# Optimization experiments

Measured on AMD Instinct MI355X. Metric: run time of the kernel, lower is better.

Reference implementation:

```python
import jax, jax.numpy as jnp
import numpy as np

EPS = 1e-5
NB, NP, NA, NROT = 16, 1024, 12, 60
C0, C1 = 64, 128
CIN, CFEAT, COUT = 256, 512, 256


def _bn(x, g, b):
    # training-mode BatchNorm1d: stats over batch (+ spatial) dims, channel dim 1
    axes = (0,) if x.ndim == 2 else (0, 2)
    m = x.mean(axis=axes, keepdims=True)
    v = x.var(axis=axes, keepdims=True)
    sh = [1] * x.ndim; sh[1] = -1
    return (x - m) * jax.lax.rsqrt(v + EPS) * g.reshape(sh) + b.reshape(sh)


def _hat(v):  # (n,3) -> (n,3,3) skew-symmetric
    z = jnp.zeros_like(v[:, 0])
    return jnp.stack([z, -v[:, 2], v[:, 1],
                      v[:, 2], z, -v[:, 0],
                      -v[:, 1], v[:, 0], z], axis=-1).reshape(-1, 3, 3)


def _exp_so3(v):  # Rodrigues formula, (n,3) -> (n,3,3)
    theta = jnp.linalg.norm(v, axis=-1, keepdims=True)  # (n,1)
    k = v / jnp.where(theta < 1e-8, 1.0, theta)
    K = _hat(k)
    s = jnp.sin(theta)[..., None]
    c = (1.0 - jnp.cos(theta))[..., None]
    I = jnp.eye(3, dtype=v.dtype)
    return I + s * K + c * (K @ K)


def _pointnet(xyz, feats, W, b, g, bb):
    # PointnetSO3Conv: concat xyz (expanded over anchors) with feats, 1x1 conv, max over points
    nb, _, npts, na = feats.shape
    x = jnp.concatenate([jnp.broadcast_to(xyz[:, :, :, None], (nb, 3, npts, na)), feats], axis=1)
    y = jnp.einsum('oc,bcpa->bopa', W, x) + b[None, :, None, None]
    y = y.max(axis=2)  # max over points -> (nb, o, na)
    return jax.nn.relu(_bn(y, g, bb))


def setup_inputs() -> dict:
    key = jax.random.key(0)
    ks = iter(jax.random.split(key, 64))
    def nrm(shape, s=0.1):
        return jax.random.normal(next(ks), shape, dtype=jnp.float32) * s
    d = {
        'xyz0': nrm((NB, 3, NP), 1.0),
        'feats0': nrm((NB, C0, NP, NA), 1.0),
        'xyz1': nrm((NB, 3, NP), 1.0),
        'feats1': nrm((NB, C1, NP, NA), 1.0),
        'trace_idx': jax.random.randint(next(ks), (NA, NROT), 0, NA),
        'anchors': nrm((NROT, 3, 3), 1.0),
        'pn0_W': nrm((C0, C0 + 3)), 'pn0_b': nrm((C0,)), 'pn0_g': jnp.ones((C0,), jnp.float32), 'pn0_bb': jnp.zeros((C0,), jnp.float32),
        'pn1_W': nrm((C1, C1 + 3)), 'pn1_b': nrm((C1,)), 'pn1_g': jnp.ones((C1,), jnp.float32), 'pn1_bb': jnp.zeros((C1,), jnp.float32),
        'lin_W': nrm((CIN, C0 + C1)), 'lin_b': nrm((CIN,)), 'lin_g': jnp.ones((CIN,), jnp.float32), 'lin_bb': jnp.zeros((CIN,), jnp.float32),
        'feat_W': nrm((CFEAT, CIN * NA)), 'feat_b': nrm((CFEAT,)), 'feat_g': jnp.ones((CFEAT,), jnp.float32), 'feat_bb': jnp.zeros((CFEAT,), jnp.float32),
        'att_W1': nrm((128, CFEAT)), 'att_b1': nrm((128,)), 'att_g': jnp.ones((128,), jnp.float32), 'att_bb': jnp.zeros((128,), jnp.float32),
        'att_W2': nrm((1, 128)), 'att_b2': nrm((1,)),
        'reg_W1': nrm((128, CFEAT)), 'reg_b1': nrm((128,)), 'reg_g': jnp.ones((128,), jnp.float32), 'reg_bb': jnp.zeros((128,), jnp.float32),
        'reg_W2': nrm((7, 128)), 'reg_b2': nrm((7,)),
        'out_W1': nrm((CFEAT, CFEAT)), 'out_b1': nrm((CFEAT,)), 'out_g': jnp.ones((CFEAT,), jnp.float32), 'out_bb': jnp.zeros((CFEAT,), jnp.float32),
        'out_W2': nrm((COUT, CFEAT)), 'out_b2': nrm((COUT,)),
    }
    return d


def reference(xyz0, feats0, xyz1, feats1, trace_idx, anchors,
              pn0_W, pn0_b, pn0_g, pn0_bb, pn1_W, pn1_b, pn1_g, pn1_bb,
              lin_W, lin_b, lin_g, lin_bb, feat_W, feat_b, feat_g, feat_bb,
              att_W1, att_b1, att_g, att_bb, att_W2, att_b2,
              reg_W1, reg_b1, reg_g, reg_bb, reg_W2, reg_b2,
              out_W1, out_b1, out_g, out_bb, out_W2, out_b2):
    nb = feats0.shape[0]
    # _pooling: per-level pointnet + BN + relu, concat, pn_linear + pn_bn
    p0 = _pointnet(xyz0, feats0, pn0_W, pn0_b, pn0_g, pn0_bb)
    p1 = _pointnet(xyz1, feats1, pn1_W, pn1_b, pn1_g, pn1_bb)
    x = jnp.concatenate([p0, p1], axis=1)                                   # (nb, 192, na)
    x = _bn(jnp.einsum('oc,bca->boa', lin_W, x) + lin_b[None, :, None], lin_g, lin_bb)  # (nb,256,na)
    # gather trace_idx_ori and flatten channel x anchor dims
    x = x[:, :, trace_idx].reshape(nb, CIN * NA, NROT)                      # (nb,3072,60)
    xf = jax.nn.relu(_bn(jnp.einsum('oc,bca->boa', feat_W, x) + feat_b[None, :, None], feat_g, feat_bb))  # (nb,512,60)
    h = jax.nn.relu(_bn(jnp.einsum('oc,bca->boa', reg_W1, xf) + reg_b1[None, :, None], reg_g, reg_bb))
    residual = (jnp.einsum('oc,bca->boa', reg_W2, h) + reg_b2[None, :, None]).transpose(0, 2, 1)  # (nb,60,7)
    res_D = residual[:, :, :3] / jnp.linalg.norm(residual[:, :, :3], axis=-1, keepdims=True)
    res_N = (jax.nn.sigmoid(residual[:, :, 3]) - 0.5) * jnp.pi / 5
    res_V = res_D * res_N[..., None]
    res_R = _exp_so3(res_V.reshape(-1, 3)).reshape(nb, NROT, 3, 3)
    res_T = residual[:, :, 4:]
    pred_R = jnp.einsum('tij,btjk->btik', anchors, res_R)
    # attention head + softmax over 60 rotations
    a = jax.nn.relu(_bn(jnp.einsum('oc,bca->boa', att_W1, xf) + att_b1[None, :, None], att_g, att_bb))
    logits = (jnp.einsum('oc,bca->boa', att_W2, a) + att_b2[None, :, None])[:, 0]   # (nb,60)
    x_attn = jax.nn.softmax(logits, axis=-1)
    # max-pool over rotations + out MLP
    xm = xf.max(axis=-1)                                                    # (nb,512)
    o = jax.nn.relu(_bn(xm @ out_W1.T + out_b1, out_g, out_bb))
    x_out = o @ out_W2.T + out_b2
    return (x_out, x_attn, pred_R, res_T)
```

## Files before the change

### kernel.cpp

```cpp
#include <hip/hip_runtime.h>
#include <math.h>

#define NBATCH 16
#define NPTS   1024
#define NANG   12
#define NROTS  60
#define EPSV   1e-5f

#define WB0_OFF   0
#define WB1_OFF   3072
#define PART0_OFF 13312
#define PART1_OFF 799744
#define XF_OFF    13312
#define XM_OFF    504832
#define OACT_OFF  513024
#define XCAT_OFF  2372608
#define XLIN_OFF  2409472
#define XG_OFF    2458624
#define BRP_OFF   2458624
#define HACT_OFF  4424704
#define AACT_OFF  4547584
#define FRAW_OFF  5407744
#define FEATW_OFF 6882304

#define OUT_XOUT 0
#define OUT_ATTN 4096
#define OUT_PRED 5056
#define OUT_REST 13696

typedef short  bf16x8 __attribute__((ext_vector_type(8)));
typedef float  f32x4  __attribute__((ext_vector_type(4)));

__device__ __forceinline__ unsigned short f2bf_rne(float x){
  unsigned int u = __float_as_uint(x);
  u += 0x7FFFu + ((u >> 16) & 1u);
  return (unsigned short)(u >> 16);
}
__device__ __forceinline__ float bf2f(unsigned short h){
  return __uint_as_float(((unsigned int)h) << 16);
}

__device__ __forceinline__ bf16x8 pack8(const float* f){
  union { unsigned int u[4]; bf16x8 v; } r;
  #pragma unroll
  for (int i = 0; i < 4; i++)
    r.u[i] = __builtin_amdgcn_perm(__float_as_uint(f[2*i+1]),
                                   __float_as_uint(f[2*i]), 0x07060302u);
  return r.v;
}

__device__ __forceinline__ void stage16(const unsigned short* g, unsigned short* l){
  __builtin_amdgcn_global_load_lds((const __attribute__((address_space(1))) void*)g,
                                   (__attribute__((address_space(3))) void*)l, 16, 0, 0);
}

template<int NT>
__device__ __forceinline__ void block_stats(float v, float& m, float& var, float* sbuf){
  constexpr int NW = NT / 64;
  float s = v, s2 = v * v;
  #pragma unroll
  for (int off = 32; off; off >>= 1){
    s  += __shfl_xor(s,  off, 64);
    s2 += __shfl_xor(s2, off, 64);
  }
  const int w = threadIdx.x >> 6;
  if ((threadIdx.x & 63) == 0){ sbuf[w] = s; sbuf[NW + w] = s2; }
  __syncthreads();
  float ts = 0.f, ts2 = 0.f;
  #pragma unroll
  for (int i = 0; i < NW; i++){ ts += sbuf[i]; ts2 += sbuf[NW + i]; }
  m = ts / (float)NT;
  var = ts2 / (float)NT - m * m;
}

template<int C>
__device__ __forceinline__ void prep_wb_body(int idx, const float* __restrict__ W,
                                             unsigned short* __restrict__ Wb){
  constexpr int KPAD = C + 32;
  if (idx >= C * KPAD) return;
  const int o = idx / KPAD, k = idx % KPAD;
  float v = 0.f;
  if (k < C)          v = W[(size_t)o * (C + 3) + 3 + k];
  else if (k < C + 3) v = W[(size_t)o * (C + 3) + (k - C)];
  Wb[idx] = f2bf_rne(v);
}

__global__ __launch_bounds__(256) void prep_all(
    const float* __restrict__ W0, const float* __restrict__ W1,
    const float* __restrict__ FW,
    unsigned short* __restrict__ wb0, unsigned short* __restrict__ wb1,
    unsigned short* __restrict__ fw2){
  const int blk = blockIdx.x;
  if (blk < 24){
    prep_wb_body<64>(blk * 256 + threadIdx.x, W0, wb0);
  } else if (blk < 104){
    prep_wb_body<128>((blk - 24) * 256 + threadIdx.x, W1, wb1);
  } else {
    const int idx = (blk - 104) * 256 + threadIdx.x;
    const int o = idx / 3072, k = idx % 3072;
    const float x = FW[idx];
    const unsigned short hi = f2bf_rne(x);
    const unsigned short lo = f2bf_rne(x - bf2f(hi));
    fw2[(size_t)o * 6144 + k] = hi;
    fw2[(size_t)o * 6144 + 3072 + k] = lo;
  }
}

#define SROW 196
template<int C>
__device__ __forceinline__ void pn_body(
    const float* __restrict__ xyz, const float* __restrict__ feats,
    const unsigned short* __restrict__ Wb, float* __restrict__ part,
    float* Bs ){
  constexpr int KPAD = C + 32;
  constexpr int NFK  = C / 32;
  constexpr int MT   = C / 16;
  const int nchunk = blockIdx.x, b = blockIdx.y;
  const int tid  = threadIdx.x;
  const int lane = tid & 63, wave = tid >> 6;
  const int g = lane >> 4, l16 = lane & 15;
  const int colbase = wave * 48;
  const int nbase   = nchunk * 192;

  int nn[3], pp[3];
  #pragma unroll
  for (int t = 0; t < 3; t++){
    nn[t] = colbase + t * 16 + l16;
    pp[t] = (nbase + nn[t]) / 12;
  }

  f32x4 acc[MT][3];
  #pragma unroll
  for (int m = 0; m < MT; m++)
    #pragma unroll
    for (int t = 0; t < 3; t++)
      acc[m][t] = (f32x4){0.f, 0.f, 0.f, 0.f};

  const float* fB = feats + (size_t)b * C * (NPTS * NANG) + nbase;

  int srow[6], scol[6], sslot[6];
  #pragma unroll
  for (int jj = 0; jj < 6; jj++){
    const int idx = tid + 256 * jj;
    srow[jj]  = idx / 48;
    scol[jj]  = (idx % 48) * 4;
    sslot[jj] = (srow[jj] & 7) * 4 + (srow[jj] >> 3);
  }

  {
    float4 v[6];
    #pragma unroll
    for (int jj = 0; jj < 6; jj++)
      v[jj] = *(const float4*)(fB + (size_t)srow[jj] * (NPTS * NANG) + scol[jj]);
    #pragma unroll
    for (int jj = 0; jj < 6; jj++)
      *(float4*)(&Bs[sslot[jj] * SROW + scol[jj]]) = v[jj];
  }
  __syncthreads();

  #pragma unroll
  for (int ks = 0; ks < NFK; ks++){
    float* Bc = Bs + (ks & 1) * (32 * SROW);
    float* Bn = Bs + ((ks & 1) ^ 1) * (32 * SROW);
    float4 v[6];
    if (ks + 1 < NFK){
      const int kb = (ks + 1) * 32;
      #pragma unroll
      for (int jj = 0; jj < 6; jj++)
        v[jj] = *(const float4*)(fB + (size_t)(kb + srow[jj]) * (NPTS * NANG) + scol[jj]);
    }
    const int kb = ks * 32;
    bf16x8 Bf[3];
    #pragma unroll
    for (int t = 0; t < 3; t++){
      float f[8];
      #pragma unroll
      for (int j = 0; j < 8; j++)
        f[j] = Bc[(j * 4 + g) * SROW + nn[t]];
      Bf[t] = pack8(f);
    }
    #pragma unroll
    for (int m = 0; m < MT; m++){
      const bf16x8 Af = *(const bf16x8*)(Wb + (size_t)(m * 16 + l16) * KPAD + kb + g * 8);
      #pragma unroll
      for (int t = 0; t < 3; t++)
        acc[m][t] = __builtin_amdgcn_mfma_f32_16x16x32_bf16(Af, Bf[t], acc[m][t], 0, 0, 0);
    }
    if (ks + 1 < NFK){
      #pragma unroll
      for (int jj = 0; jj < 6; jj++)
        *(float4*)(&Bn[sslot[jj] * SROW + scol[jj]]) = v[jj];
    }
    __syncthreads();
  }

  {
    const int kb = C;
    bf16x8 Bf[3];
    #pragma unroll
    for (int t = 0; t < 3; t++){
      float f[8];
      #pragma unroll
      for (int j = 0; j < 8; j++) f[j] = 0.f;
      if (g == 0){
        #pragma unroll
        for (int j = 0; j < 3; j++)
          f[j] = xyz[(size_t)(b * 3 + j) * NPTS + pp[t]];
      }
      Bf[t] = pack8(f);
    }
    #pragma unroll
    for (int m = 0; m < MT; m++){
      const bf16x8 Af = *(const bf16x8*)(Wb + (size_t)(m * 16 + l16) * KPAD + kb + g * 8);
      #pragma unroll
      for (int t = 0; t < 3; t++)
        acc[m][t] = __builtin_amdgcn_mfma_f32_16x16x32_bf16(Af, Bf[t], acc[m][t], 0, 0, 0);
    }
  }

  float* yb = Bs;
  #pragma unroll
  for (int m = 0; m < MT; m++){
    __syncthreads();
    #pragma unroll
    for (int t = 0; t < 3; t++)
      #pragma unroll
      for (int r = 0; r < 4; r++)
        yb[(g * 4 + r) * SROW + nn[t]] = acc[m][t][r];
    __syncthreads();
    if (tid < 192){
      const int o_l = tid / 12, a = tid % 12;
      float mx = -3.4e38f;
      #pragma unroll
      for (int pl = 0; pl < 16; pl++)
        mx = fmaxf(mx, yb[o_l * SROW + pl * 12 + a]);
      part[((size_t)(b * 64 + nchunk) * C + m * 16 + o_l) * 12 + a] = mx;
    }
  }
}

__global__ __launch_bounds__(256) void pn_both(
    const float* __restrict__ xyz0, const float* __restrict__ feats0,
    const unsigned short* __restrict__ wb0, float* __restrict__ part0,
    const float* __restrict__ xyz1, const float* __restrict__ feats1,
    const unsigned short* __restrict__ wb1, float* __restrict__ part1){
  __shared__ float Bs[2 * 32 * SROW];
  if (blockIdx.z == 0) pn_body<64> (xyz0, feats0, wb0, part0, Bs);
  else                 pn_body<128>(xyz1, feats1, wb1, part1, Bs);
}

__global__ void pn_reduce_bn(const float* __restrict__ part0, const float* __restrict__ part1,
    const float* __restrict__ b0, const float* __restrict__ g0, const float* __restrict__ bb0,
    const float* __restrict__ b1, const float* __restrict__ g1, const float* __restrict__ bb1,
    float* __restrict__ xcat){
  const int ch = blockIdx.x, t = threadIdx.x;
  const int b = t / 12, a = t % 12;
  const float* part; const float *bias, *g, *bb; int o, Cl;
  if (ch < 64){ part = part0; bias = b0; g = g0; bb = bb0; o = ch;      Cl = 64;  }
  else        { part = part1; bias = b1; g = g1; bb = bb1; o = ch - 64; Cl = 128; }
  const float* pp = part + ((size_t)(b * 64) * Cl + o) * 12 + a;
  const size_t kstride = (size_t)Cl * 12;
  float v = pp[0];
  for (int k = 1; k < 64; k++) v = fmaxf(v, pp[(size_t)k * kstride]);
  v += bias[o];
  __shared__ float sbuf[8];
  float m, var;
  block_stats<192>(v, m, var, sbuf);
  float xn = (v - m) * rsqrtf(var + EPSV) * g[o] + bb[o];
  xcat[((size_t)b * 192 + ch) * 12 + a] = fmaxf(xn, 0.f);
}

__global__ void lin_bn(const float* __restrict__ xcat, const float* __restrict__ W,
    const float* __restrict__ bias, const float* __restrict__ g, const float* __restrict__ bb,
    float* __restrict__ xlin){
  const int o = blockIdx.x, t = threadIdx.x;
  const int b = t / 12, a = t % 12;
  const float* xr = xcat + (size_t)b * 2304 + a;
  const float* wr = W + (size_t)o * 192;
  float v = bias[o];
  for (int c = 0; c < 192; c++) v = fmaf(wr[c], xr[(size_t)c * 12], v);
  __shared__ float sbuf[8];
  float m, var;
  block_stats<192>(v, m, var, sbuf);
  xlin[((size_t)b * 256 + o) * 12 + a] = (v - m) * rsqrtf(var + EPSV) * g[o] + bb[o];
}

__global__ void prep_xg(const float* __restrict__ xlin, const int* __restrict__ trace,
                        unsigned short* __restrict__ Xg){
  const int n = blockIdx.x;
  const int b = n / 60, r = n % 60;
  unsigned short* row = Xg + (size_t)n * 6144;
  __shared__ int ta[12];
  if (threadIdx.x < 12) ta[threadIdx.x] = trace[threadIdx.x * 60 + r];
  __syncthreads();
  for (int i = threadIdx.x; i < 3072; i += 256){
    const int c = i / 12, a = i % 12;
    const float x = xlin[((size_t)b * 256 + c) * 12 + ta[a]];
    const unsigned short hi = f2bf_rne(x);
    const unsigned short lo = f2bf_rne(x - bf2f(hi));
    row[i] = hi;
    row[3072 + i] = lo;
  }
}

__global__ __launch_bounds__(256) void feat_mfma(
    const unsigned short* __restrict__ Wb2, const unsigned short* __restrict__ Xg,
    float* __restrict__ fraw){
  const int nblk = blockIdx.x, mblk = blockIdx.y, seg = blockIdx.z;
  const int tid = threadIdx.x;
  const int lane = tid & 63, wave = tid >> 6;
  const int g = lane >> 4, l16 = lane & 15;
  const int kA = (seg == 1) ? 3072 : 0;
  const int kB = (seg == 2) ? 3072 : 0;
  const int sw = l16 & 7;
  const int wm = wave >> 1, wn = wave & 1;

  __shared__ unsigned short As[2][64 * 64];
  __shared__ unsigned short Bs[2][64 * 64];

  int rowj[2], colj[2], ldsoff[2];
  #pragma unroll
  for (int j = 0; j < 2; j++){
    const int idx = j * 256 + wave * 64 + lane;
    rowj[j]   = idx >> 3;
    colj[j]   = ((idx & 7) ^ (rowj[j] & 7)) * 8;
    ldsoff[j] = (j * 256 + wave * 64) * 8;
  }
  const unsigned short* Agb = Wb2 + (size_t)mblk * 64 * 6144 + kA;
  const unsigned short* Bgb = Xg  + (size_t)nblk * 64 * 6144 + kB;

  f32x4 acc[2][2];
  #pragma unroll
  for (int i = 0; i < 2; i++)
    #pragma unroll
    for (int j = 0; j < 2; j++)
      acc[i][j] = (f32x4){0.f, 0.f, 0.f, 0.f};

  #pragma unroll
  for (int j = 0; j < 2; j++){
    stage16(Agb + (size_t)rowj[j] * 6144 + colj[j], &As[0][ldsoff[j]]);
    stage16(Bgb + (size_t)rowj[j] * 6144 + colj[j], &Bs[0][ldsoff[j]]);
  }
  __syncthreads();

  for (int kc = 0; kc < 3072; kc += 64){
    const int buf = (kc >> 6) & 1;
    if (kc + 64 < 3072){
      const int kn = kc + 64;
      #pragma unroll
      for (int j = 0; j < 2; j++){
        stage16(Agb + (size_t)rowj[j] * 6144 + kn + colj[j], &As[buf ^ 1][ldsoff[j]]);
        stage16(Bgb + (size_t)rowj[j] * 6144 + kn + colj[j], &Bs[buf ^ 1][ldsoff[j]]);
      }
    }
    #pragma unroll
    for (int kc2 = 0; kc2 < 64; kc2 += 32){
      const int c0 = kc2 >> 3;
      bf16x8 af[2], bfr[2];
      #pragma unroll
      for (int i = 0; i < 2; i++)
        af[i]  = *(const bf16x8*)&As[buf][(wm * 32 + i * 16 + l16) * 64 + ((c0 + g) ^ sw) * 8];
      #pragma unroll
      for (int i = 0; i < 2; i++)
        bfr[i] = *(const bf16x8*)&Bs[buf][(wn * 32 + i * 16 + l16) * 64 + ((c0 + g) ^ sw) * 8];
      #pragma unroll
      for (int i = 0; i < 2; i++)
        #pragma unroll
        for (int j = 0; j < 2; j++)
          acc[i][j] = __builtin_amdgcn_mfma_f32_16x16x32_bf16(af[i], bfr[j], acc[i][j], 0, 0, 0);
    }
    __syncthreads();
  }

  float* base = fraw + (size_t)seg * (512 * 960);
  #pragma unroll
  for (int i = 0; i < 2; i++)
    #pragma unroll
    for (int j = 0; j < 2; j++){
      const int n = nblk * 64 + wn * 32 + j * 16 + l16;
      #pragma unroll
      for (int q = 0; q < 4; q++){
        const int m = mblk * 64 + wm * 32 + i * 16 + g * 4 + q;
        base[(size_t)m * 960 + n] = acc[i][j][q];
      }
    }
}

__global__ void feat_bn(const float* __restrict__ fraw, const float* __restrict__ bias,
    const float* __restrict__ g, const float* __restrict__ bb,
    float* __restrict__ xf, float* __restrict__ xm){
  const int o = blockIdx.x, t = threadIdx.x;
  const int b = t / 60, r = t % 60;
  const size_t SS = (size_t)512 * 960;
  const size_t in = (size_t)o * 960 + t;
  float v = fraw[in] + fraw[SS + in] + fraw[2 * SS + in] + bias[o];
  __shared__ float sbuf[32];
  float m, var;
  block_stats<960>(v, m, var, sbuf);
  const float xn = fmaxf((v - m) * rsqrtf(var + EPSV) * g[o] + bb[o], 0.f);
  xf[((size_t)b * 512 + o) * 60 + r] = xn;
  __shared__ float red[960];
  red[t] = xn;
  __syncthreads();
  if (r == 0){
    float mx = red[t];
    for (int k = 1; k < 60; k++) mx = fmaxf(mx, red[t + k]);
    xm[(size_t)b * 512 + o] = mx;
  }
}

__global__ __launch_bounds__(256) void brgemm_oh1(const float* __restrict__ xf,
    const float* __restrict__ Wr, const float* __restrict__ Wa,
    float* __restrict__ brp,
    const float* __restrict__ xm, const float* __restrict__ oW1,
    const float* __restrict__ ob1, const float* __restrict__ og,
    const float* __restrict__ obb, float* __restrict__ o_act){
  const int z = blockIdx.z;
  if (z == 16){
    const int q = blockIdx.y * 4 + blockIdx.x;
    if (q >= 32) return;
    const int t = threadIdx.x;
    const int b = t & 15, j = t >> 4;
    const int oc = q * 16 + j;
    float acc = ob1[oc];
    const float* wr = oW1 + (size_t)oc * 512;
    const float* xr = xm + (size_t)b * 512;
    for (int c = 0; c < 512; c++) acc = fmaf(wr[c], xr[c], acc);
    float s = acc, s2 = acc * acc;
    #pragma unroll
    for (int off = 8; off; off >>= 1){
      s  += __shfl_xor(s,  off, 16);
      s2 += __shfl_xor(s2, off, 16);
    }
    const float m = s * (1.f / 16.f);
    const float var = s2 * (1.f / 16.f) - m * m;
    o_act[(size_t)b * 512 + oc] = fmaxf((acc - m) * rsqrtf(var + EPSV) * og[oc] + obb[oc], 0.f);
    return;
  }
  const int og_ = blockIdx.x, b = blockIdx.y;
  const int br = z >> 3, ks = z & 7;
  const float* W = br ? Wa : Wr;
  const int lane = threadIdx.x & 63, wave = threadIdx.x >> 6;
  const int obase = og_ * 32 + wave * 8;
  const int rr = lane < 60 ? lane : 0;
  const float* xb = xf + ((size_t)b * 512 + ks * 64) * 60 + rr;
  const float* wr = W + (size_t)obase * 512 + ks * 64;

  float acc[8];
  #pragma unroll
  for (int i = 0; i < 8; i++) acc[i] = 0.f;

  float cur[4], nxt[4];
  #pragma unroll
  for (int j = 0; j < 4; j++) cur[j] = xb[(size_t)j * 60];

  for (int c0 = 0; c0 < 64; c0 += 4){
    #pragma unroll
    for (int j = 0; j < 4; j++){
      int cc = c0 + 4 + j; if (cc > 63) cc = 63;
      nxt[j] = xb[(size_t)cc * 60];
    }
    #pragma unroll
    for (int j = 0; j < 4; j++)
      #pragma unroll
      for (int i = 0; i < 8; i++)
        acc[i] = fmaf(wr[(size_t)i * 512 + c0 + j], cur[j], acc[i]);
    #pragma unroll
    for (int j = 0; j < 4; j++) cur[j] = nxt[j];
  }

  if (lane < 60){
    #pragma unroll
    for (int i = 0; i < 8; i++)
      brp[(((size_t)z * NBATCH + b) * 128 + obase + i) * 60 + lane] = acc[i];
  }
}

__global__ void br_bn(const float* __restrict__ brp,
    const float* __restrict__ biasR, const float* __restrict__ gR, const float* __restrict__ bbR,
    const float* __restrict__ biasA, const float* __restrict__ gA, const float* __restrict__ bbA,
    float* __restrict__ hact, float* __restrict__ aact){
  const int o = blockIdx.x, br = blockIdx.y, t = threadIdx.x;
  const int b = t / 60, r = t % 60;
  const float* bias = br ? biasA : biasR;
  const float* g    = br ? gA    : gR;
  const float* bb   = br ? bbA   : bbR;
  float v = bias[o];
  #pragma unroll
  for (int ks = 0; ks < 8; ks++)
    v += brp[((((size_t)br * 8 + ks) * NBATCH + b) * 128 + o) * 60 + r];
  __shared__ float sbuf[32];
  float m, var;
  block_stats<960>(v, m, var, sbuf);
  float* outp = br ? aact : hact;
  outp[((size_t)b * 128 + o) * 60 + r] =
      fmaxf((v - m) * rsqrtf(var + EPSV) * g[o] + bb[o], 0.f);
}

__global__ void heads(
    const float* __restrict__ h, const float* __restrict__ rW2,
    const float* __restrict__ rb2, const float* __restrict__ anchors,
    const float* __restrict__ a, const float* __restrict__ aW2, const float* __restrict__ ab2,
    const float* __restrict__ o_act, const float* __restrict__ oW2,
    const float* __restrict__ ob2, float* __restrict__ out){
  const int b = blockIdx.x, sel = blockIdx.y, t = threadIdx.x;
  if (sel == 0){
    if (t >= 64) return;
    const int r = t < 60 ? t : 59;
    float res[7];
    #pragma unroll
    for (int j = 0; j < 7; j++) res[j] = rb2[j];
    for (int c = 0; c < 128; c++){
      const float hv = h[((size_t)b * 128 + c) * 60 + r];
      #pragma unroll
      for (int j = 0; j < 7; j++) res[j] = fmaf(rW2[j * 128 + c], hv, res[j]);
    }
    if (t >= 60) return;
    const float n = sqrtf(res[0]*res[0] + res[1]*res[1] + res[2]*res[2]);
    const float invn = 1.f / n;
    const float Nv = (1.f / (1.f + expf(-res[3])) - 0.5f) * 3.14159265358979323846f / 5.f;
    const float v0 = res[0]*invn*Nv, v1 = res[1]*invn*Nv, v2 = res[2]*invn*Nv;
    const float th = sqrtf(v0*v0 + v1*v1 + v2*v2);
    const float invt = th < 1e-8f ? 1.f : 1.f / th;
    const float k0 = v0*invt, k1 = v1*invt, k2 = v2*invt;
    const float s = sinf(th), cc = 1.f - cosf(th);
    const float K[9] = {0.f, -k2, k1,  k2, 0.f, -k0,  -k1, k0, 0.f};
    float K2[9];
    #pragma unroll
    for (int ii = 0; ii < 3; ii++)
      #pragma unroll
      for (int jj = 0; jj < 3; jj++)
        K2[ii*3+jj] = K[ii*3+0]*K[0*3+jj] + K[ii*3+1]*K[1*3+jj] + K[ii*3+2]*K[2*3+jj];
    float R[9];
    #pragma unroll
    for (int ii = 0; ii < 3; ii++)
      #pragma unroll
      for (int jj = 0; jj < 3; jj++)
        R[ii*3+jj] = (ii == jj ? 1.f : 0.f) + s * K[ii*3+jj] + cc * K2[ii*3+jj];
    const float* A = anchors + (size_t)t * 9;
    #pragma unroll
    for (int ii = 0; ii < 3; ii++)
      #pragma unroll
      for (int kk = 0; kk < 3; kk++){
        const float pv = A[ii*3+0]*R[0*3+kk] + A[ii*3+1]*R[1*3+kk] + A[ii*3+2]*R[2*3+kk];
        out[OUT_PRED + ((size_t)b * 60 + t) * 9 + ii * 3 + kk] = pv;
      }
    #pragma unroll
    for (int k = 0; k < 3; k++)
      out[OUT_REST + ((size_t)b * 60 + t) * 3 + k] = res[4 + k];
  } else if (sel == 1){
    if (t >= 64) return;
    const int r = t < 60 ? t : 59;
    float acc = ab2[0];
    for (int c = 0; c < 128; c++)
      acc = fmaf(aW2[c], a[((size_t)b * 128 + c) * 60 + r], acc);
    const float l = t < 60 ? acc : -INFINITY;
    float mx = l;
    #pragma unroll
    for (int off = 32; off; off >>= 1) mx = fmaxf(mx, __shfl_xor(mx, off, 64));
    const float e = t < 60 ? expf(l - mx) : 0.f;
    float ssum = e;
    #pragma unroll
    for (int off = 32; off; off >>= 1) ssum += __shfl_xor(ssum, off, 64);
    if (t < 60) out[OUT_ATTN + (size_t)b * 60 + t] = e / ssum;
  } else {
    const float* wr = oW2 + (size_t)t * 512;
    const float* xr = o_act + (size_t)b * 512;
    float acc = ob2[t];
    for (int c = 0; c < 512; c++) acc = fmaf(wr[c], xr[c], acc);
    out[OUT_XOUT + (size_t)b * 256 + t] = acc;
  }
}

extern "C" void kernel_launch(void* const* d_in, const int* in_sizes, int n_in,
                              void* d_out, int out_size, void* d_ws, size_t ws_size,
                              hipStream_t stream){
  const float* xyz0    = (const float*)d_in[0];
  const float* feats0  = (const float*)d_in[1];
  const float* xyz1    = (const float*)d_in[2];
  const float* feats1  = (const float*)d_in[3];
  const int*   trace   = (const int*)  d_in[4];
  const float* anchors = (const float*)d_in[5];
  const float* pn0_W  = (const float*)d_in[6];
  const float* pn0_b  = (const float*)d_in[7];
  const float* pn0_g  = (const float*)d_in[8];
  const float* pn0_bb = (const float*)d_in[9];
  const float* pn1_W  = (const float*)d_in[10];
  const float* pn1_b  = (const float*)d_in[11];
  const float* pn1_g  = (const float*)d_in[12];
  const float* pn1_bb = (const float*)d_in[13];
  const float* lin_W  = (const float*)d_in[14];
  const float* lin_b  = (const float*)d_in[15];
  const float* lin_g  = (const float*)d_in[16];
  const float* lin_bb = (const float*)d_in[17];
  const float* feat_W  = (const float*)d_in[18];
  const float* feat_b  = (const float*)d_in[19];
  const float* feat_g  = (const float*)d_in[20];
  const float* feat_bb = (const float*)d_in[21];
  const float* att_W1 = (const float*)d_in[22];
  const float* att_b1 = (const float*)d_in[23];
  const float* att_g  = (const float*)d_in[24];
  const float* att_bb = (const float*)d_in[25];
  const float* att_W2 = (const float*)d_in[26];
  const float* att_b2 = (const float*)d_in[27];
  const float* reg_W1 = (const float*)d_in[28];
  const float* reg_b1 = (const float*)d_in[29];
  const float* reg_g  = (const float*)d_in[30];
  const float* reg_bb = (const float*)d_in[31];
  const float* reg_W2 = (const float*)d_in[32];
  const float* reg_b2 = (const float*)d_in[33];
  const float* out_W1 = (const float*)d_in[34];
  const float* out_b1 = (const float*)d_in[35];
  const float* out_g  = (const float*)d_in[36];
  const float* out_bb = (const float*)d_in[37];
  const float* out_W2 = (const float*)d_in[38];
  const float* out_b2 = (const float*)d_in[39];

  float* ws  = (float*)d_ws;
  float* out = (float*)d_out;
  unsigned short* wb0 = (unsigned short*)(ws + WB0_OFF);
  unsigned short* wb1 = (unsigned short*)(ws + WB1_OFF);
  unsigned short* fw  = (unsigned short*)(ws + FEATW_OFF);
  unsigned short* xg  = (unsigned short*)(ws + XG_OFF);

  prep_all<<<6248, 256, 0, stream>>>(pn0_W, pn1_W, feat_W, wb0, wb1, fw);

  pn_both<<<dim3(64, 16, 2), 256, 0, stream>>>(xyz0, feats0, wb0, ws + PART0_OFF,
                                               xyz1, feats1, wb1, ws + PART1_OFF);

  pn_reduce_bn<<<192, 192, 0, stream>>>(ws + PART0_OFF, ws + PART1_OFF,
      pn0_b, pn0_g, pn0_bb, pn1_b, pn1_g, pn1_bb, ws + XCAT_OFF);

  lin_bn<<<256, 192, 0, stream>>>(ws + XCAT_OFF, lin_W, lin_b, lin_g, lin_bb, ws + XLIN_OFF);

  prep_xg<<<960, 256, 0, stream>>>(ws + XLIN_OFF, trace, xg);

  feat_mfma<<<dim3(15, 8, 3), 256, 0, stream>>>(fw, xg, ws + FRAW_OFF);

  feat_bn<<<512, 960, 0, stream>>>(ws + FRAW_OFF, feat_b, feat_g, feat_bb,
                                   ws + XF_OFF, ws + XM_OFF);

  brgemm_oh1<<<dim3(4, 16, 17), 256, 0, stream>>>(ws + XF_OFF, reg_W1, att_W1, ws + BRP_OFF,
      ws + XM_OFF, out_W1, out_b1, out_g, out_bb, ws + OACT_OFF);

  br_bn<<<dim3(128, 2), 960, 0, stream>>>(ws + BRP_OFF,
      reg_b1, reg_g, reg_bb, att_b1, att_g, att_bb,
      ws + HACT_OFF, ws + AACT_OFF);

  heads<<<dim3(16, 3), 256, 0, stream>>>(ws + HACT_OFF, reg_W2, reg_b2, anchors,
      ws + AACT_OFF, att_W2, att_b2, ws + OACT_OFF, out_W2, out_b2, out);
}
```

Before: 431.1 us.

## Load PointNet B-operand directly from global, drop LDS staging, interleave block types

```diff
diff --git a/kernel.cpp b/kernel.cpp
--- a/kernel.cpp
+++ b/kernel.cpp
@@ -109,23 +109,22 @@
 #define SROW 196
 template<int C>
 __device__ __forceinline__ void pn_body(
+    int nchunk, int b,
     const float* __restrict__ xyz, const float* __restrict__ feats,
     const unsigned short* __restrict__ Wb, float* __restrict__ part,
-    float* Bs ){
+    float* yb ){
   constexpr int KPAD = C + 32;
   constexpr int NFK  = C / 32;
   constexpr int MT   = C / 16;
-  const int nchunk = blockIdx.x, b = blockIdx.y;
   const int tid  = threadIdx.x;
   const int lane = tid & 63, wave = tid >> 6;
   const int g = lane >> 4, l16 = lane & 15;
-  const int colbase = wave * 48;
-  const int nbase   = nchunk * 192;
+  const int nbase = nchunk * 192;
 
   int nn[3], pp[3];
   #pragma unroll
   for (int t = 0; t < 3; t++){
-    nn[t] = colbase + t * 16 + l16;
+    nn[t] = wave * 48 + t * 16 + l16;
     pp[t] = (nbase + nn[t]) / 12;
   }
 
@@ -138,47 +137,18 @@
 
   const float* fB = feats + (size_t)b * C * (NPTS * NANG) + nbase;
 
-  int srow[6], scol[6], sslot[6];
-  #pragma unroll
-  for (int jj = 0; jj < 6; jj++){
-    const int idx = tid + 256 * jj;
-    srow[jj]  = idx / 48;
-    scol[jj]  = (idx % 48) * 4;
-    sslot[jj] = (srow[jj] & 7) * 4 + (srow[jj] >> 3);
-  }
-
-  {
-    float4 v[6];
-    #pragma unroll
-    for (int jj = 0; jj < 6; jj++)
-      v[jj] = *(const float4*)(fB + (size_t)srow[jj] * (NPTS * NANG) + scol[jj]);
-    #pragma unroll
-    for (int jj = 0; jj < 6; jj++)
-      *(float4*)(&Bs[sslot[jj] * SROW + scol[jj]]) = v[jj];
-  }
-  __syncthreads();
-
   #pragma unroll
   for (int ks = 0; ks < NFK; ks++){
-    float* Bc = Bs + (ks & 1) * (32 * SROW);
-    float* Bn = Bs + ((ks & 1) ^ 1) * (32 * SROW);
-    float4 v[6];
-    if (ks + 1 < NFK){
-      const int kb = (ks + 1) * 32;
-      #pragma unroll
-      for (int jj = 0; jj < 6; jj++)
-        v[jj] = *(const float4*)(fB + (size_t)(kb + srow[jj]) * (NPTS * NANG) + scol[jj]);
-    }
     const int kb = ks * 32;
+    float f[3][8];
+    #pragma unroll
+    for (int t = 0; t < 3; t++)
+      #pragma unroll
+      for (int j = 0; j < 8; j++)
+        f[t][j] = fB[(size_t)(kb + g * 8 + j) * (NPTS * NANG) + nn[t]];
     bf16x8 Bf[3];
     #pragma unroll
-    for (int t = 0; t < 3; t++){
-      float f[8];
-      #pragma unroll
-      for (int j = 0; j < 8; j++)
-        f[j] = Bc[(j * 4 + g) * SROW + nn[t]];
-      Bf[t] = pack8(f);
-    }
+    for (int t = 0; t < 3; t++) Bf[t] = pack8(f[t]);
     #pragma unroll
     for (int m = 0; m < MT; m++){
       const bf16x8 Af = *(const bf16x8*)(Wb + (size_t)(m * 16 + l16) * KPAD + kb + g * 8);
@@ -186,12 +156,6 @@
       for (int t = 0; t < 3; t++)
         acc[m][t] = __builtin_amdgcn_mfma_f32_16x16x32_bf16(Af, Bf[t], acc[m][t], 0, 0, 0);
     }
-    if (ks + 1 < NFK){
-      #pragma unroll
-      for (int jj = 0; jj < 6; jj++)
-        *(float4*)(&Bn[sslot[jj] * SROW + scol[jj]]) = v[jj];
-    }
-    __syncthreads();
   }
 
   {
@@ -218,7 +182,6 @@
     }
   }
 
-  float* yb = Bs;
   #pragma unroll
   for (int m = 0; m < MT; m++){
     __syncthreads();
@@ -239,14 +202,18 @@
   }
 }
 
-__global__ __launch_bounds__(256) void pn_both(
+__global__ __launch_bounds__(256, 3) void pn_both(
     const float* __restrict__ xyz0, const float* __restrict__ feats0,
     const unsigned short* __restrict__ wb0, float* __restrict__ part0,
     const float* __restrict__ xyz1, const float* __restrict__ feats1,
     const unsigned short* __restrict__ wb1, float* __restrict__ part1){
-  __shared__ float Bs[2 * 32 * SROW];
-  if (blockIdx.z == 0) pn_body<64> (xyz0, feats0, wb0, part0, Bs);
-  else                 pn_body<128>(xyz1, feats1, wb1, part1, Bs);
+  __shared__ float yb[16 * SROW];
+  const int lin   = blockIdx.x + 64 * (blockIdx.y + 16 * blockIdx.z);
+  const int which = lin & 1;
+  const int rest  = lin >> 1;
+  const int nchunk = rest & 63, b = rest >> 6;
+  if (which == 0) pn_body<64> (nchunk, b, xyz0, feats0, wb0, part0, yb);
+  else            pn_body<128>(nchunk, b, xyz1, feats1, wb1, part1, yb);
 }
 
 __global__ void pn_reduce_bn(const float* __restrict__ part0, const float* __restrict__ part1,
```

After: 438.0 us. About the same (+1.6%).
